# Optimization experiments

Hardware: AMD Instinct MI355X
Metric: run time of the kernel (lower is better)

## Reference

```python
import jax, jax.numpy as jnp
import numpy as np

N = 50000      # nodes
E = 800000     # edges (before self-loops)
F_IN = 128     # args.nsegment
H = 4          # args.nhead
C = 32         # args.dhidden
OUT = 64       # output_dim
G = 64         # number of graphs in batch
NEG = 0.2      # args.negslope (and GATv2 internal leaky-relu slope, PyG default 0.2)


def setup_inputs() -> dict:
    key = jax.random.key(0)
    ks = jax.random.split(key, 8)
    def w(k, i, o):
        return jax.random.normal(k, (i, o), jnp.float32) / np.sqrt(i)
    x = jax.random.normal(ks[0], (N, F_IN), jnp.float32)
    edge_index = jax.random.randint(ks[1], (2, E), 0, N, dtype=jnp.int32)
    batch = jnp.sort(jax.random.randint(ks[2], (N,), 0, G, dtype=jnp.int32))
    d = dict(x=x, edge_index=edge_index, batch=batch)
    # layer dims: (in_dim, heads, out_per_head, concat)
    dims = [(F_IN, H, C, True), (H * C, H, C, True), (H * C, 1, OUT, False)]
    for li, (fi, h, c, concat) in enumerate(dims):
        k1, k2, k3 = jax.random.split(ks[3 + li], 3)
        d[f"Wl{li}"] = w(k1, fi, h * c)
        d[f"Wr{li}"] = w(k2, fi, h * c)
        d[f"att{li}"] = jax.random.normal(k3, (h, c), jnp.float32) / np.sqrt(c)
        d[f"b{li}"] = jnp.zeros((h * c if concat else c,), jnp.float32)
    return d


def _gat_layer(x, src, tgt, Wl, Wr, att, b, concat):
    """GATv2Conv: e_ij = att . leaky_relu(Wl x_j + Wr x_i); softmax over edges into i;
    out_i = sum_j alpha_ij * (Wl x_j). src/tgt include self-loops."""
    n = x.shape[0]
    h, c = att.shape
    xl = (x @ Wl).reshape(n, h, c)                 # source transform [N,h,c]
    xr = (x @ Wr).reshape(n, h, c)                 # target transform [N,h,c]
    g = jax.nn.leaky_relu(xl[src] + xr[tgt], NEG)  # [Etot,h,c]
    score = jnp.einsum('ehc,hc->eh', g, att)       # [Etot,h]
    smax = jax.ops.segment_max(score, tgt, num_segments=n)
    ex = jnp.exp(score - smax[tgt])
    den = jax.ops.segment_sum(ex, tgt, num_segments=n)
    alpha = ex / den[tgt]                          # per-target softmax [Etot,h]
    out = jax.ops.segment_sum(xl[src] * alpha[:, :, None], tgt, num_segments=n)
    out = out.reshape(n, h * c) if concat else out.mean(axis=1)
    return out + b


def _forward(x, edge_index, batch, params):
    n = x.shape[0]
    loops = jnp.arange(n, dtype=edge_index.dtype)  # PyG add_self_loops=True
    src = jnp.concatenate([edge_index[0], loops])
    tgt = jnp.concatenate([edge_index[1], loops])
    for Wl, Wr, att, b, concat in params:
        x = _gat_layer(x, src, tgt, Wl, Wr, att, b, concat)
        x = jax.nn.leaky_relu(x, NEG)  # dropout p is identity in eval mode
    ssum = jax.ops.segment_sum(x, batch, num_segments=G)
    cnt = jax.ops.segment_sum(jnp.ones((n,), x.dtype), batch, num_segments=G)
    return ssum / jnp.maximum(cnt, 1.0)[:, None]   # global_mean_pool -> [G, OUT]


def reference(x, edge_index, batch, Wl0, Wr0, att0, b0, Wl1, Wr1, att1, b1, Wl2, Wr2, att2, b2):
    params = [(Wl0, Wr0, att0, b0, True),
              (Wl1, Wr1, att1, b1, True),
              (Wl2, Wr2, att2, b2, False)]
    return _forward(x, edge_index, batch, params)
```

## Files before the change

kernel.cpp:

```cpp
#include <hip/hip_runtime.h>
#include <hip/hip_fp16.h>
#include <math.h>

#define NEGSLOPE 0.2f

typedef _Float16 f16x8 __attribute__((ext_vector_type(8)));
typedef float f32x4 __attribute__((ext_vector_type(4)));

__device__ __forceinline__ float lrelu(float x) { return x > 0.f ? x : NEGSLOPE * x; }

__global__ void k_count(const int* __restrict__ tgt, int* __restrict__ deg, int e) {
    int i = blockIdx.x * 256 + threadIdx.x;
    if (i < e) atomicAdd(&deg[tgt[i]], 1);
}
__global__ __launch_bounds__(256) void k_scanA(const int* __restrict__ deg, int* __restrict__ rowptr,
                                               int* __restrict__ bsums, int n) {
    __shared__ int s[256];
    int t = threadIdx.x;
    int base = blockIdx.x * 4096 + t * 16;
    int pre[16];
    int sum = 0;
    for (int i = 0; i < 16; ++i) {
        int idx = base + i;
        int v = (idx < n) ? (deg[idx] + 1) : 0;
        pre[i] = sum;
        sum += v;
    }
    s[t] = sum;
    __syncthreads();
    for (int off = 1; off < 256; off <<= 1) {
        int v = (t >= off) ? s[t - off] : 0;
        __syncthreads();
        s[t] += v;
        __syncthreads();
    }
    int tbase = s[t] - sum;
    for (int i = 0; i < 16; ++i) {
        int idx = base + i;
        if (idx < n) rowptr[idx] = tbase + pre[i];
    }
    if (t == 0) bsums[blockIdx.x] = s[255];
}
__global__ void k_scanB(int* __restrict__ bsums, int* __restrict__ rowptr, int nblk, int n) {
    if (threadIdx.x == 0 && blockIdx.x == 0) {
        int run = 0;
        for (int i = 0; i < nblk; ++i) { int v = bsums[i]; bsums[i] = run; run += v; }
        rowptr[n] = run;
    }
}
__global__ void k_scanC(int* __restrict__ rowptr, const int* __restrict__ bsums,
                        int* __restrict__ edst, int* __restrict__ cursor, int n) {
    int i = blockIdx.x * 256 + threadIdx.x;
    if (i < n) {
        int rp = rowptr[i] + bsums[i >> 12];
        rowptr[i] = rp;
        edst[rp] = i;
        cursor[i] = rp + 1;
    }
}
__global__ void k_scatter(const int* __restrict__ src, const int* __restrict__ tgt,
                          int* __restrict__ cursor, int* __restrict__ edst, int e) {
    int i = blockIdx.x * 256 + threadIdx.x;
    if (i < e) { int p = atomicAdd(&cursor[tgt[i]], 1); edst[p] = src[i]; }
}

__global__ void k_xconv(const float* __restrict__ x, _Float16* __restrict__ xh, int n8) {
    int i = blockIdx.x * 256 + threadIdx.x;
    if (i < n8) {
        float4 a = ((const float4*)x)[2 * i], b = ((const float4*)x)[2 * i + 1];
        union { uint4 u; _Float16 h[8]; } pk;
        pk.h[0] = (_Float16)a.x; pk.h[1] = (_Float16)a.y;
        pk.h[2] = (_Float16)a.z; pk.h[3] = (_Float16)a.w;
        pk.h[4] = (_Float16)b.x; pk.h[5] = (_Float16)b.y;
        pk.h[6] = (_Float16)b.z; pk.h[7] = (_Float16)b.w;
        ((uint4*)xh)[i] = pk.u;
    }
}
__global__ void k_wconv(const float* W0, const float* W1, const float* W2,
                        const float* W3, const float* W4, const float* W5,
                        _Float16* D0, _Float16* D1, _Float16* D2,
                        _Float16* D3, _Float16* D4, _Float16* D5) {
    int b = blockIdx.x, k = threadIdx.x;
    const float* src; _Float16* dst; int col, kout;
    if (b < 128)      { src = W0; dst = D0; col = b;       kout = 128; }
    else if (b < 256) { src = W1; dst = D1; col = b - 128; kout = 128; }
    else if (b < 384) { src = W2; dst = D2; col = b - 256; kout = 128; }
    else if (b < 512) { src = W3; dst = D3; col = b - 384; kout = 128; }
    else if (b < 576) { src = W4; dst = D4; col = b - 512; kout = 64; }
    else              { src = W5; dst = D5; col = b - 576; kout = 64; }
    dst[col * 128 + k] = (_Float16)src[k * kout + col];
}

template<int KOUT>
__global__ __launch_bounds__(256) void k_gemm_mfma(
        const _Float16* __restrict__ Ah,
        const _Float16* __restrict__ Wt0, const _Float16* __restrict__ Wt1,
        _Float16* __restrict__ out0, float* __restrict__ out1, int n) {
    int wv = threadIdx.x >> 6, lane = threadIdx.x & 63;
    int m = lane & 15, q = lane >> 4;
    int row0 = blockIdx.x * 64 + wv * 16;
    int arow = row0 + m; if (arow >= n) arow = n - 1;
    const _Float16* ap = Ah + (size_t)arow * 128 + q * 8;
    f16x8 af[4];
#pragma unroll
    for (int kt = 0; kt < 4; ++kt) af[kt] = *(const f16x8*)(ap + 32 * kt);

    f32x4 acc[8] = {};
    const _Float16* Wsel = Wt0;
    if (KOUT == 128 && blockIdx.y) Wsel = Wt1;
#pragma unroll
    for (int kt = 0; kt < 4; ++kt) {
#pragma unroll
        for (int ct = 0; ct < 8; ++ct) {
            const _Float16* W = (KOUT == 128) ? Wsel : (ct < 4 ? Wt0 : Wt1);
            int col0 = (KOUT == 128) ? ct * 16 : (ct & 3) * 16;
            f16x8 bf = *(const f16x8*)(W + (size_t)(col0 + m) * 128 + 32 * kt + 8 * q);
            acc[ct] = __builtin_amdgcn_mfma_f32_16x16x32_f16(af[kt], bf, acc[ct], 0, 0, 0);
        }
    }
#pragma unroll
    for (int ct = 0; ct < 8; ++ct) {
        bool asHalf = (KOUT == 128) ? (blockIdx.y == 0) : (ct < 4);
        int col0 = (KOUT == 128) ? ct * 16 : (ct & 3) * 16;
        int col = col0 + m;
#pragma unroll
        for (int i = 0; i < 4; ++i) {
            int r = row0 + q * 4 + i;
            if (r < n) {
                if (asHalf) out0[(size_t)r * KOUT + col] = (_Float16)acc[ct][i];
                else        out1[(size_t)r * KOUT + col] = acc[ct][i];
            }
        }
    }
}

template<int H, int C, typename OutT>
__global__ __launch_bounds__(256) void k_agg(const __half* __restrict__ xl, const float* __restrict__ xr,
                                             const float* __restrict__ att, const float* __restrict__ bias,
                                             const int* __restrict__ rowptr, const int* __restrict__ edst,
                                             OutT* __restrict__ yout, int n) {
    constexpr int F = H * C;
    constexpr int VEC = F / 16;
    constexpr int L = C / VEC;
    int lane = threadIdx.x & 63;
    int wave = threadIdx.x >> 6;
    int s = lane & 15;
    int node = blockIdx.x * 16 + wave * 4 + (lane >> 4);
    bool valid = node < n;
    int nodeSafe = valid ? node : 0;
    int ch = s * VEC;

    float u[VEC], av[VEC], acc[VEC];
#pragma unroll
    for (int j = 0; j < VEC; ++j) {
        u[j] = xr[(size_t)nodeSafe * F + ch + j];
        av[j] = att[ch + j];
        acc[j] = 0.f;
    }
    int e0 = rowptr[nodeSafe];
    int deg = valid ? (rowptr[nodeSafe + 1] - e0) : 0;
    int maxdeg = deg;
    maxdeg = max(maxdeg, __shfl_xor(maxdeg, 16));
    maxdeg = max(maxdeg, __shfl_xor(maxdeg, 32));
    float ssum = 0.f;

    auto loadrow = [&](int src, float* v) {
        const __half* p = xl + (size_t)src * F + ch;
        if constexpr (VEC == 8) {
            union { uint4 u4; __half2 h[4]; } pk;
            pk.u4 = *(const uint4*)p;
#pragma unroll
            for (int j = 0; j < 4; ++j) {
                float2 f = __half22float2(pk.h[j]);
                v[2 * j] = f.x; v[2 * j + 1] = f.y;
            }
        } else {
            union { uint2 u2; __half2 h[2]; } pk;
            pk.u2 = *(const uint2*)p;
#pragma unroll
            for (int j = 0; j < 2; ++j) {
                float2 f = __half22float2(pk.h[j]);
                v[2 * j] = f.x; v[2 * j + 1] = f.y;
            }
        }
    };
    auto dot = [&](const float* v) {
        float p = 0.f;
#pragma unroll
        for (int j = 0; j < VEC; ++j) p += lrelu(v[j] + u[j]) * av[j];
        return p;
    };
    auto accum = [&](float w, const float* v) {
        ssum += w;
#pragma unroll
        for (int j = 0; j < VEC; ++j) acc[j] += w * v[j];
    };

    for (int base = 0; base < maxdeg; base += 16) {
        int cnt = deg - base;
        if (cnt > 16) cnt = 16;
        int idxreg = (s < cnt) ? edst[e0 + base + s] : nodeSafe;
        int mcnt = cnt;
        mcnt = max(mcnt, __shfl_xor(mcnt, 16));
        mcnt = max(mcnt, __shfl_xor(mcnt, 32));
        int gbase = lane & 48;
        int i = 0;
        for (; i + 4 <= mcnt; i += 4) {
            int s0 = __shfl(idxreg, gbase + i);
            int s1 = __shfl(idxreg, gbase + i + 1);
            int s2 = __shfl(idxreg, gbase + i + 2);
            int s3 = __shfl(idxreg, gbase + i + 3);
            float v0[VEC], v1[VEC], v2[VEC], v3[VEC];
            loadrow(s0, v0); loadrow(s1, v1); loadrow(s2, v2); loadrow(s3, v3);
            float p0 = dot(v0), p1 = dot(v1), p2 = dot(v2), p3 = dot(v3);
#pragma unroll
            for (int off = 1; off < L; off <<= 1) {
                p0 += __shfl_xor(p0, off);
                p1 += __shfl_xor(p1, off);
                p2 += __shfl_xor(p2, off);
                p3 += __shfl_xor(p3, off);
            }
            float w0 = (i + 0 < cnt) ? __expf(p0) : 0.f;
            float w1 = (i + 1 < cnt) ? __expf(p1) : 0.f;
            float w2 = (i + 2 < cnt) ? __expf(p2) : 0.f;
            float w3 = (i + 3 < cnt) ? __expf(p3) : 0.f;
            accum(w0, v0); accum(w1, v1); accum(w2, v2); accum(w3, v3);
        }
        for (; i < mcnt; ++i) {
            int s0 = __shfl(idxreg, gbase + i);
            float v[VEC];
            loadrow(s0, v);
            float p = dot(v);
#pragma unroll
            for (int off = 1; off < L; off <<= 1) p += __shfl_xor(p, off);
            float w = (i < cnt) ? __expf(p) : 0.f;
            accum(w, v);
        }
    }
    if (valid) {
        float inv = 1.f / ssum;
        float o[VEC];
#pragma unroll
        for (int j = 0; j < VEC; ++j) o[j] = lrelu(acc[j] * inv + bias[ch + j]);
        if constexpr (sizeof(OutT) == 2) {
            _Float16* p = (_Float16*)yout + (size_t)node * F + ch;
            if constexpr (VEC == 8) {
                union { uint4 u; _Float16 h[8]; } pk;
#pragma unroll
                for (int j = 0; j < 8; ++j) pk.h[j] = (_Float16)o[j];
                *(uint4*)p = pk.u;
            } else {
                union { uint2 u; _Float16 h[4]; } pk;
#pragma unroll
                for (int j = 0; j < 4; ++j) pk.h[j] = (_Float16)o[j];
                *(uint2*)p = pk.u;
            }
        } else {
            float* p = (float*)yout + (size_t)node * F + ch;
            *(float4*)p = make_float4(o[0], o[1], o[2], o[3]);
            if constexpr (VEC == 8)
                *(float4*)(p + 4) = make_float4(o[4], o[5], o[6], o[7]);
        }
    }
}

__global__ __launch_bounds__(256) void k_pool_partial(const float* __restrict__ y,
        const int* __restrict__ batch, float* __restrict__ pacc, int n, int nchunk) {
    __shared__ float sdata[256];
    __shared__ int range[2];
    int g = blockIdx.x;
    int chunk = blockIdx.y;
    int t = threadIdx.x;
    if (t == 0) {
        int lo = 0, hi = n;
        while (lo < hi) { int mid = (lo + hi) >> 1; if (batch[mid] < g) lo = mid + 1; else hi = mid; }
        range[0] = lo;
        hi = n;
        while (lo < hi) { int mid = (lo + hi) >> 1; if (batch[mid] < g + 1) lo = mid + 1; else hi = mid; }
        range[1] = lo;
    }
    __syncthreads();
    int start = range[0], len = range[1] - range[0];
    int lo = start + (int)((long long)len * chunk / nchunk);
    int hi = start + (int)((long long)len * (chunk + 1) / nchunk);
    int ch = t & 63, sub = t >> 6;
    float acc = 0.f;
    for (int node = lo + sub; node < hi; node += 4)
        acc += y[(size_t)node * 64 + ch];
    sdata[t] = acc;
    __syncthreads();
    if (t < 128) sdata[t] += sdata[t + 128];
    __syncthreads();
    if (t < 64) atomicAdd(&pacc[g * 64 + t], sdata[t] + sdata[t + 64]);
}
__global__ void k_pool_final(const float* __restrict__ pacc, const int* __restrict__ batch,
                             float* __restrict__ out, int n) {
    __shared__ int cntS;
    int g = blockIdx.x, t = threadIdx.x;
    if (t == 0) {
        int lo = 0, hi = n;
        while (lo < hi) { int mid = (lo + hi) >> 1; if (batch[mid] < g) lo = mid + 1; else hi = mid; }
        int s = lo;
        hi = n;
        while (lo < hi) { int mid = (lo + hi) >> 1; if (batch[mid] < g + 1) lo = mid + 1; else hi = mid; }
        cntS = lo - s;
    }
    __syncthreads();
    out[g * 64 + t] = pacc[g * 64 + t] / fmaxf((float)cntS, 1.f);
}

extern "C" void kernel_launch(void* const* d_in, const int* in_sizes, int n_in,
                              void* d_out, int out_size, void* d_ws, size_t ws_size,
                              hipStream_t stream) {
    const float* x     = (const float*)d_in[0];
    const int*   ei    = (const int*)d_in[1];
    const int*   batch = (const int*)d_in[2];
    const float* Wl0 = (const float*)d_in[3];
    const float* Wr0 = (const float*)d_in[4];
    const float* att0 = (const float*)d_in[5];
    const float* b0  = (const float*)d_in[6];
    const float* Wl1 = (const float*)d_in[7];
    const float* Wr1 = (const float*)d_in[8];
    const float* att1 = (const float*)d_in[9];
    const float* b1  = (const float*)d_in[10];
    const float* Wl2 = (const float*)d_in[11];
    const float* Wr2 = (const float*)d_in[12];
    const float* att2 = (const float*)d_in[13];
    const float* b2  = (const float*)d_in[14];

    const int N = in_sizes[2];
    const int E = in_sizes[1] / 2;
    const int G = out_size / 64;
    const int* src = ei;
    const int* tgt = ei + E;

    size_t off = 0;
    auto take = [&](size_t bytes) {
        void* p = (char*)d_ws + off;
        off = (off + bytes + 255) & ~(size_t)255;
        return p;
    };
    _Float16* xh   = (_Float16*)take((size_t)N * 128 * 2);
    _Float16* Ah   = (_Float16*)take((size_t)N * 128 * 2);
    float* B       = (float*)take((size_t)N * 128 * 4);
    _Float16* Cbh  = (_Float16*)take((size_t)N * 128 * 2);
    float* Cbf     = (float*)take((size_t)N * 64 * 4);
    _Float16* Wl0t = (_Float16*)take(128 * 128 * 2);
    _Float16* Wr0t = (_Float16*)take(128 * 128 * 2);
    _Float16* Wl1t = (_Float16*)take(128 * 128 * 2);
    _Float16* Wr1t = (_Float16*)take(128 * 128 * 2);
    _Float16* Wl2t = (_Float16*)take(64 * 128 * 2);
    _Float16* Wr2t = (_Float16*)take(64 * 128 * 2);
    int* rowptr = (int*)take((size_t)(N + 1) * 4);
    int* tmp    = (int*)take((size_t)N * 4);
    float* pacc = (float*)take((size_t)G * 64 * 4);
    int* edst   = (int*)take((size_t)(E + N) * 4);
    int* bsums  = (int*)take(64 * 4);
    (void)ws_size; (void)n_in;

    const int TB = 256;
    int nblkN = (N + TB - 1) / TB;
    int nblkE = (E + TB - 1) / TB;
    int nscan = (N + 4095) / 4096;

    hipMemsetAsync(tmp, 0, (size_t)((char*)(pacc + G * 64) - (char*)tmp), stream);

    k_count<<<nblkE, TB, 0, stream>>>(tgt, tmp, E);
    k_scanA<<<nscan, TB, 0, stream>>>(tmp, rowptr, bsums, N);
    k_scanB<<<1, 64, 0, stream>>>(bsums, rowptr, nscan, N);
    k_scanC<<<nblkN, TB, 0, stream>>>(rowptr, bsums, edst, tmp, N);
    k_scatter<<<nblkE, TB, 0, stream>>>(src, tgt, tmp, edst, E);

    k_xconv<<<(N * 128 / 8 + TB - 1) / TB, TB, 0, stream>>>(x, xh, N * 128 / 8);
    k_wconv<<<640, 128, 0, stream>>>(Wl0, Wr0, Wl1, Wr1, Wl2, Wr2,
                                     Wl0t, Wr0t, Wl1t, Wr1t, Wl2t, Wr2t);

    int gemmBlocks = (N + 63) / 64;
    dim3 gemmGrid2(gemmBlocks, 2);
    dim3 gemmGrid1(gemmBlocks, 1);
    int aggBlocks = (N + 15) / 16;

    k_gemm_mfma<128><<<gemmGrid2, TB, 0, stream>>>(xh, Wl0t, Wr0t, Ah, B, N);
    k_agg<4, 32, _Float16><<<aggBlocks, TB, 0, stream>>>((const __half*)Ah, B, att0, b0, rowptr, edst, Cbh, N);

    k_gemm_mfma<128><<<gemmGrid2, TB, 0, stream>>>(Cbh, Wl1t, Wr1t, Ah, B, N);
    k_agg<4, 32, _Float16><<<aggBlocks, TB, 0, stream>>>((const __half*)Ah, B, att1, b1, rowptr, edst, Cbh, N);

    k_gemm_mfma<64><<<gemmGrid1, TB, 0, stream>>>(Cbh, Wl2t, Wr2t, Ah, B, N);
    k_agg<1, 64, float><<<aggBlocks, TB, 0, stream>>>((const __half*)Ah, B, att2, b2, rowptr, edst, Cbf, N);

    dim3 poolGrid(G, 16);
    k_pool_partial<<<poolGrid, TB, 0, stream>>>(Cbf, batch, pacc, N, 16);
    k_pool_final<<<G, 64, 0, stream>>>(pacc, batch, (float*)d_out, N);
}
```

Measured before the change: 412.9 us.

## Fuse prep kernels, use atomic ranks for CSR scatter, merge GEMM halves

Merges the x conversion, weight transpose and zeroing memset into one prep kernel, and folds the serial block-sum scan into scanC. The count kernel now records each edge's atomic rank, so the scatter writes to a computed position with a nontemporal store instead of doing a second atomic. The 128-wide GEMM now computes both Wl and Wr outputs in one block rather than splitting them across grid.y, which reuses the A fragments but doubles accumulators per wave. Together these cut launches and atomics, at the cost of an extra rank buffer and more register pressure in the GEMM.

Result: faster. 404.1 us (-2.1%).

```diff
diff --git a/kernel.cpp b/kernel.cpp
--- a/kernel.cpp
+++ b/kernel.cpp
@@ -9,9 +9,45 @@
 
 __device__ __forceinline__ float lrelu(float x) { return x > 0.f ? x : NEGSLOPE * x; }
 
-__global__ void k_count(const int* __restrict__ tgt, int* __restrict__ deg, int e) {
+__global__ __launch_bounds__(256) void k_prep(
+        const float* __restrict__ x, _Float16* __restrict__ xh, int n8, int XB,
+        const float* W0, const float* W1, const float* W2,
+        const float* W3, const float* W4, const float* W5,
+        _Float16* D0, _Float16* D1, _Float16* D2,
+        _Float16* D3, _Float16* D4, _Float16* D5,
+        int* __restrict__ deg, float* __restrict__ pacc, int n, int npacc) {
+    int b = blockIdx.x, t = threadIdx.x;
+    if (b < XB) {
+        int i = b * 256 + t;
+        if (i < n8) {
+            float4 a = ((const float4*)x)[2 * i], c = ((const float4*)x)[2 * i + 1];
+            union { uint4 u; _Float16 h[8]; } pk;
+            pk.h[0] = (_Float16)a.x; pk.h[1] = (_Float16)a.y;
+            pk.h[2] = (_Float16)a.z; pk.h[3] = (_Float16)a.w;
+            pk.h[4] = (_Float16)c.x; pk.h[5] = (_Float16)c.y;
+            pk.h[6] = (_Float16)c.z; pk.h[7] = (_Float16)c.w;
+            ((uint4*)xh)[i] = pk.u;
+        }
+    } else if (b < XB + 320) {
+        const float* Ws[6] = {W0, W1, W2, W3, W4, W5};
+        _Float16* Ds[6] = {D0, D1, D2, D3, D4, D5};
+        int j = (b - XB) * 256 + t;
+        int m, jj, kout;
+        if (j < 65536) { m = j >> 14; jj = j & 16383; kout = 128; }
+        else           { m = 4 + ((j - 65536) >> 13); jj = (j - 65536) & 8191; kout = 64; }
+        int col = jj >> 7, k = jj & 127;
+        Ds[m][col * 128 + k] = (_Float16)Ws[m][k * kout + col];
+    } else {
+        int i = (b - XB - 320) * 256 + t;
+        if (i < n) deg[i] = 0;
+        else if (i < n + npacc) pacc[i - n] = 0.f;
+    }
+}
+
+__global__ void k_count(const int* __restrict__ tgt, int* __restrict__ deg,
+                        int* __restrict__ rank, int e) {
     int i = blockIdx.x * 256 + threadIdx.x;
-    if (i < e) atomicAdd(&deg[tgt[i]], 1);
+    if (i < e) rank[i] = atomicAdd(&deg[tgt[i]], 1);
 }
 __global__ __launch_bounds__(256) void k_scanA(const int* __restrict__ deg, int* __restrict__ rowptr,
                                                int* __restrict__ bsums, int n) {
@@ -41,54 +77,32 @@
     }
     if (t == 0) bsums[blockIdx.x] = s[255];
 }
-__global__ void k_scanB(int* __restrict__ bsums, int* __restrict__ rowptr, int nblk, int n) {
-    if (threadIdx.x == 0 && blockIdx.x == 0) {
+__global__ __launch_bounds__(256) void k_scanC(int* __restrict__ rowptr, const int* __restrict__ bsums,
+                                               int* __restrict__ edst, int nscan, int n) {
+    __shared__ int pref[65];
+    int t = threadIdx.x;
+    if (t == 0) {
         int run = 0;
-        for (int i = 0; i < nblk; ++i) { int v = bsums[i]; bsums[i] = run; run += v; }
-        rowptr[n] = run;
-    }
-}
-__global__ void k_scanC(int* __restrict__ rowptr, const int* __restrict__ bsums,
-                        int* __restrict__ edst, int* __restrict__ cursor, int n) {
-    int i = blockIdx.x * 256 + threadIdx.x;
+        for (int k = 0; k < nscan; ++k) { pref[k] = run; run += bsums[k]; }
+        pref[nscan] = run;
+    }
+    __syncthreads();
+    int i = blockIdx.x * 256 + t;
     if (i < n) {
-        int rp = rowptr[i] + bsums[i >> 12];
+        int rp = rowptr[i] + pref[i >> 12];
         rowptr[i] = rp;
         edst[rp] = i;
-        cursor[i] = rp + 1;
-    }
+    }
+    if (blockIdx.x == gridDim.x - 1 && t == 0) rowptr[n] = pref[nscan];
 }
 __global__ void k_scatter(const int* __restrict__ src, const int* __restrict__ tgt,
-                          int* __restrict__ cursor, int* __restrict__ edst, int e) {
+                          const int* __restrict__ rank, const int* __restrict__ rowptr,
+                          int* __restrict__ edst, int e) {
     int i = blockIdx.x * 256 + threadIdx.x;
-    if (i < e) { int p = atomicAdd(&cursor[tgt[i]], 1); edst[p] = src[i]; }
-}
-
-__global__ void k_xconv(const float* __restrict__ x, _Float16* __restrict__ xh, int n8) {
-    int i = blockIdx.x * 256 + threadIdx.x;
-    if (i < n8) {
-        float4 a = ((const float4*)x)[2 * i], b = ((const float4*)x)[2 * i + 1];
-        union { uint4 u; _Float16 h[8]; } pk;
-        pk.h[0] = (_Float16)a.x; pk.h[1] = (_Float16)a.y;
-        pk.h[2] = (_Float16)a.z; pk.h[3] = (_Float16)a.w;
-        pk.h[4] = (_Float16)b.x; pk.h[5] = (_Float16)b.y;
-        pk.h[6] = (_Float16)b.z; pk.h[7] = (_Float16)b.w;
-        ((uint4*)xh)[i] = pk.u;
-    }
-}
-__global__ void k_wconv(const float* W0, const float* W1, const float* W2,
-                        const float* W3, const float* W4, const float* W5,
-                        _Float16* D0, _Float16* D1, _Float16* D2,
-                        _Float16* D3, _Float16* D4, _Float16* D5) {
-    int b = blockIdx.x, k = threadIdx.x;
-    const float* src; _Float16* dst; int col, kout;
-    if (b < 128)      { src = W0; dst = D0; col = b;       kout = 128; }
-    else if (b < 256) { src = W1; dst = D1; col = b - 128; kout = 128; }
-    else if (b < 384) { src = W2; dst = D2; col = b - 256; kout = 128; }
-    else if (b < 512) { src = W3; dst = D3; col = b - 384; kout = 128; }
-    else if (b < 576) { src = W4; dst = D4; col = b - 512; kout = 64; }
-    else              { src = W5; dst = D5; col = b - 576; kout = 64; }
-    dst[col * 128 + k] = (_Float16)src[k * kout + col];
+    if (i < e) {
+        int p = rowptr[tgt[i]] + 1 + rank[i];
+        __builtin_nontemporal_store(src[i], &edst[p]);
+    }
 }
 
 template<int KOUT>
@@ -96,6 +110,7 @@
         const _Float16* __restrict__ Ah,
         const _Float16* __restrict__ Wt0, const _Float16* __restrict__ Wt1,
         _Float16* __restrict__ out0, float* __restrict__ out1, int n) {
+    constexpr int CT = KOUT / 16;
     int wv = threadIdx.x >> 6, lane = threadIdx.x & 63;
     int m = lane & 15, q = lane >> 4;
     int row0 = blockIdx.x * 64 + wv * 16;
@@ -105,24 +120,21 @@
 #pragma unroll
     for (int kt = 0; kt < 4; ++kt) af[kt] = *(const f16x8*)(ap + 32 * kt);
 
-    f32x4 acc[8] = {};
-    const _Float16* Wsel = Wt0;
-    if (KOUT == 128 && blockIdx.y) Wsel = Wt1;
+    f32x4 acc[2 * CT] = {};
 #pragma unroll
     for (int kt = 0; kt < 4; ++kt) {
 #pragma unroll
-        for (int ct = 0; ct < 8; ++ct) {
-            const _Float16* W = (KOUT == 128) ? Wsel : (ct < 4 ? Wt0 : Wt1);
-            int col0 = (KOUT == 128) ? ct * 16 : (ct & 3) * 16;
+        for (int ct = 0; ct < 2 * CT; ++ct) {
+            const _Float16* W = (ct < CT) ? Wt0 : Wt1;
+            int col0 = (ct % CT) * 16;
             f16x8 bf = *(const f16x8*)(W + (size_t)(col0 + m) * 128 + 32 * kt + 8 * q);
             acc[ct] = __builtin_amdgcn_mfma_f32_16x16x32_f16(af[kt], bf, acc[ct], 0, 0, 0);
         }
     }
 #pragma unroll
-    for (int ct = 0; ct < 8; ++ct) {
-        bool asHalf = (KOUT == 128) ? (blockIdx.y == 0) : (ct < 4);
-        int col0 = (KOUT == 128) ? ct * 16 : (ct & 3) * 16;
-        int col = col0 + m;
+    for (int ct = 0; ct < 2 * CT; ++ct) {
+        bool asHalf = (ct < CT);
+        int col = (ct % CT) * 16 + m;
 #pragma unroll
         for (int i = 0; i < 4; ++i) {
             int r = row0 + q * 4 + i;
@@ -354,6 +366,7 @@
     int* rowptr = (int*)take((size_t)(N + 1) * 4);
     int* tmp    = (int*)take((size_t)N * 4);
     float* pacc = (float*)take((size_t)G * 64 * 4);
+    int* rank   = (int*)take((size_t)E * 4);
     int* edst   = (int*)take((size_t)(E + N) * 4);
     int* bsums  = (int*)take(64 * 4);
     (void)ws_size; (void)n_in;
@@ -363,30 +376,29 @@
     int nblkE = (E + TB - 1) / TB;
     int nscan = (N + 4095) / 4096;
 
-    hipMemsetAsync(tmp, 0, (size_t)((char*)(pacc + G * 64) - (char*)tmp), stream);
-
-    k_count<<<nblkE, TB, 0, stream>>>(tgt, tmp, E);
+    int n8 = N * 128 / 8;
+    int XB = (n8 + TB - 1) / TB;
+    int ZB = (N + G * 64 + TB - 1) / TB;
+    k_prep<<<XB + 320 + ZB, TB, 0, stream>>>(x, xh, n8, XB,
+        Wl0, Wr0, Wl1, Wr1, Wl2, Wr2,
+        Wl0t, Wr0t, Wl1t, Wr1t, Wl2t, Wr2t,
+        tmp, pacc, N, G * 64);
+
+    k_count<<<nblkE, TB, 0, stream>>>(tgt, tmp, rank, E);
     k_scanA<<<nscan, TB, 0, stream>>>(tmp, rowptr, bsums, N);
-    k_scanB<<<1, 64, 0, stream>>>(bsums, rowptr, nscan, N);
-    k_scanC<<<nblkN, TB, 0, stream>>>(rowptr, bsums, edst, tmp, N);
-    k_scatter<<<nblkE, TB, 0, stream>>>(src, tgt, tmp, edst, E);
-
-    k_xconv<<<(N * 128 / 8 + TB - 1) / TB, TB, 0, stream>>>(x, xh, N * 128 / 8);
-    k_wconv<<<640, 128, 0, stream>>>(Wl0, Wr0, Wl1, Wr1, Wl2, Wr2,
-                                     Wl0t, Wr0t, Wl1t, Wr1t, Wl2t, Wr2t);
+    k_scanC<<<nblkN, TB, 0, stream>>>(rowptr, bsums, edst, nscan, N);
+    k_scatter<<<nblkE, TB, 0, stream>>>(src, tgt, rank, rowptr, edst, E);
 
     int gemmBlocks = (N + 63) / 64;
-    dim3 gemmGrid2(gemmBlocks, 2);
-    dim3 gemmGrid1(gemmBlocks, 1);
     int aggBlocks = (N + 15) / 16;
 
-    k_gemm_mfma<128><<<gemmGrid2, TB, 0, stream>>>(xh, Wl0t, Wr0t, Ah, B, N);
+    k_gemm_mfma<128><<<gemmBlocks, TB, 0, stream>>>(xh, Wl0t, Wr0t, Ah, B, N);
     k_agg<4, 32, _Float16><<<aggBlocks, TB, 0, stream>>>((const __half*)Ah, B, att0, b0, rowptr, edst, Cbh, N);
 
-    k_gemm_mfma<128><<<gemmGrid2, TB, 0, stream>>>(Cbh, Wl1t, Wr1t, Ah, B, N);
+    k_gemm_mfma<128><<<gemmBlocks, TB, 0, stream>>>(Cbh, Wl1t, Wr1t, Ah, B, N);
     k_agg<4, 32, _Float16><<<aggBlocks, TB, 0, stream>>>((const __half*)Ah, B, att1, b1, rowptr, edst, Cbh, N);
 
-    k_gemm_mfma<64><<<gemmGrid1, TB, 0, stream>>>(Cbh, Wl2t, Wr2t, Ah, B, N);
+    k_gemm_mfma<64><<<gemmBlocks, TB, 0, stream>>>(Cbh, Wl2t, Wr2t, Ah, B, N);
     k_agg<1, 64, float><<<aggBlocks, TB, 0, stream>>>((const __half*)Ah, B, att2, b2, rowptr, edst, Cbf, N);
 
     dim3 poolGrid(G, 16);
```
